# Kernel optimization log

Hardware: AMD Instinct MI355X
Metric: run time of the kernel (lower is better)

## Reference

```python
import jax, jax.numpy as jnp
import numpy as np

H = 2048      # hidden_size
NH = 16       # num_heads
HD = H // NH  # attention_head_size = 128
NEG_BIAS = -10000.0


def setup_inputs() -> dict:
    key = jax.random.key(0)
    k1, k2, k3, k4, k5 = jax.random.split(key, 5)
    B, S = 2, 2048
    hidden_states = jax.random.normal(k1, (B, S, H), dtype=jnp.float32)
    scale = 1.0 / np.sqrt(H)
    w_qkv = jax.random.normal(k2, (H, 3 * H), dtype=jnp.float32) * scale
    b_qkv = jax.random.normal(k3, (3 * H,), dtype=jnp.float32) * 0.01
    w_out = jax.random.normal(k4, (H, H), dtype=jnp.float32) * scale
    b_out = jax.random.normal(k5, (H,), dtype=jnp.float32) * 0.01
    return {"hidden_states": hidden_states, "w_qkv": w_qkv, "b_qkv": b_qkv,
            "w_out": w_out, "b_out": b_out}


def reference(hidden_states, w_qkv, b_qkv, w_out, b_out):
    B, S, _ = hidden_states.shape
    # fused QKV projection -> [B, S, 3H]
    qkv = hidden_states @ w_qkv + b_qkv
    # split heads with 3*head_dim per head, then chunk (matches torch code)
    qkv = qkv.reshape(B, S, NH, 3 * HD).transpose(0, 2, 1, 3)  # [B, NH, S, 3*HD]
    q, k, v = jnp.split(qkv, 3, axis=-1)                       # each [B, NH, S, HD]
    # scaled scores [B, NH, S, S]
    scores = jnp.einsum('bhqd,bhkd->bhqk', q, k) / np.sqrt(HD)
    causal = jnp.tril(jnp.ones((S, S), dtype=bool))
    scores = jnp.where(causal[None, None], scores, jnp.float32(NEG_BIAS))
    probs = jax.nn.softmax(scores, axis=-1)
    ctx = jnp.einsum('bhqk,bhkd->bhqd', probs, v)  # [B, NH, S, HD]
    ctx = ctx.transpose(0, 2, 1, 3).reshape(B, S, H)
    return ctx @ w_out + b_out
```

## Files before the change

kernel.cpp:

```cpp
#include <hip/hip_runtime.h>
#include <hip/hip_bf16.h>

typedef __bf16 bf16x8 __attribute__((ext_vector_type(8)));
typedef float  f32x4  __attribute__((ext_vector_type(4)));

constexpr int   Bb   = 2;
constexpr int   Slen = 2048;
constexpr int   Hdim = 2048;
constexpr int   NHn  = 16;
constexpr int   HDd  = 128;
constexpr float QSCALE = 0.08838834764831845f;
constexpr float NEG    = -1e30f;

__device__ __forceinline__ void gld16(const __bf16* g, __bf16* l) {
    __builtin_amdgcn_global_load_lds(
        (__attribute__((address_space(1))) void*)(uintptr_t)(const void*)g,
        (__attribute__((address_space(3))) void*)l, 16, 0, 0);
}

__global__ __launch_bounds__(256) void cvt_bf16(const float* __restrict__ in,
                                                __bf16* __restrict__ out) {
    const size_t i = (size_t)(blockIdx.x * 256 + threadIdx.x) * 8;
    f32x4 a = *(const f32x4*)(in + i), b = *(const f32x4*)(in + i + 4);
    bf16x8 r;
    r[0] = (__bf16)a[0]; r[1] = (__bf16)a[1]; r[2] = (__bf16)a[2]; r[3] = (__bf16)a[3];
    r[4] = (__bf16)b[0]; r[5] = (__bf16)b[1]; r[6] = (__bf16)b[2]; r[7] = (__bf16)b[3];
    *(bf16x8*)(out + i) = r;
}

__global__ __launch_bounds__(256) void transpose_cvt(const float* __restrict__ in,
                                                     __bf16* __restrict__ out,
                                                     int R, int C) {
    __shared__ float t[64][65];
    const int c0 = blockIdx.x * 64, r0 = blockIdx.y * 64;
    const int tx = threadIdx.x & 63, ty = threadIdx.x >> 6;
#pragma unroll
    for (int i = 0; i < 16; ++i) {
        int r = i * 4 + ty;
        t[r][tx] = in[(size_t)(r0 + r) * C + c0 + tx];
    }
    __syncthreads();
#pragma unroll
    for (int i = 0; i < 16; ++i) {
        int r = i * 4 + ty;
        out[(size_t)(c0 + r) * R + r0 + tx] = (__bf16)t[tx][r];
    }
}


#define BAR    __builtin_amdgcn_s_barrier()
#define LGKM0  asm volatile("s_waitcnt lgkmcnt(0)" ::: "memory")
#define VMC(n) asm volatile("s_waitcnt vmcnt(" #n ")" ::: "memory")

#define STAGE(op, half, tt)                                                          \
  do {                                                                               \
    const int tt_ = (tt);                                                            \
    if (tt_ < NT) {                                                                  \
      __bf16* dst_ = lds + ((tt_ & 1) << 15) + ((op) << 14) + ((half) << 13);        \
      const __bf16* src_ = (op) ? Bt : A;                                            \
      const int rb_ = (op) ? n0 : m0;                                               \
      const int k0_ = tt_ << 6;                                                      \
      _Pragma("unroll")                                                              \
      for (int i_ = 0; i_ < 2; ++i_) {                                               \
        const int c_  = (i_ << 9) + tid;                                             \
        const int rl_ = c_ >> 3;                                                     \
        const int grow_ = rb_ + ((op) ? (((rl_ >> 5) << 6) + ((half) << 5) + (rl_ & 31)) \
                                      : (((rl_ >> 6) << 7) + ((half) << 6) + (rl_ & 63))); \
        const int gk_ = k0_ + (((c_ & 7) ^ (rl_ & 7)) << 3);                         \
        gld16(src_ + (size_t)grow_ * Kdim + gk_, dst_ + (c_ << 3));                  \
      }                                                                              \
    }                                                                                \
  } while (0)

#define LDA(bufv, mh)                                                                \
  do {                                                                               \
    const __bf16* Ab_ = lds + ((bufv) << 15) + ((mh) << 13) + (wg << 12) + (l16 << 6); \
    _Pragma("unroll")                                                                \
    for (int q_ = 0; q_ < 4; ++q_)                                                   \
      _Pragma("unroll")                                                              \
      for (int kk_ = 0; kk_ < 2; ++kk_)                                              \
        af[q_][kk_] = *(const bf16x8*)(Ab_ + (q_ << 10) +                            \
                        ((((kk_ << 2) + quad) ^ (l16 & 7)) << 3));                   \
  } while (0)

#define LDB(bufv, nh)                                                                \
  do {                                                                               \
    const __bf16* Bb_ = lds + ((bufv) << 15) + 16384 + ((nh) << 13) + (gn << 11) + (l16 << 6); \
    _Pragma("unroll")                                                                \
    for (int q_ = 0; q_ < 2; ++q_)                                                   \
      _Pragma("unroll")                                                              \
      for (int kk_ = 0; kk_ < 2; ++kk_)                                              \
        bfr[((nh) << 1) + q_][kk_] = *(const bf16x8*)(Bb_ + (q_ << 10) +             \
                        ((((kk_ << 2) + quad) ^ (l16 & 7)) << 3));                   \
  } while (0)

#define MM(mh, nh)                                                                   \
  do {                                                                               \
    _Pragma("unroll")                                                                \
    for (int q_ = 0; q_ < 4; ++q_)                                                   \
      _Pragma("unroll")                                                              \
      for (int n_ = 0; n_ < 2; ++n_)                                                 \
        _Pragma("unroll")                                                            \
        for (int kk_ = 0; kk_ < 2; ++kk_)                                            \
          acc[((mh) << 2) + q_][((nh) << 1) + n_] =                                  \
            __builtin_amdgcn_mfma_f32_16x16x32_bf16(                                 \
              af[q_][kk_], bfr[((nh) << 1) + n_][kk_],                               \
              acc[((mh) << 2) + q_][((nh) << 1) + n_], 0, 0, 0);                     \
  } while (0)

template <int MODE>
__global__ __launch_bounds__(512, 2) void gemm8(
    const __bf16* __restrict__ A, const __bf16* __restrict__ Bt,
    const float* __restrict__ bias, int Kdim, int Ndim,
    float* __restrict__ Cout,
    __bf16* __restrict__ Qo, __bf16* __restrict__ Ko, __bf16* __restrict__ Vto) {
    __shared__ __bf16 lds[65536];
    const int tid  = threadIdx.x;
    const int lane = tid & 63, wave = tid >> 6;
    const int quad = lane >> 4, l16 = lane & 15;
    const int wg = wave >> 2;
    const int gn = wave & 3;
    const int m0 = blockIdx.y * 256, n0 = blockIdx.x * 256;
    const int NT = Kdim >> 6;

    f32x4  acc[8][4] = {};
    bf16x8 af[4][2];
    bf16x8 bfr[4][2];

    STAGE(0, 0, 0); STAGE(1, 0, 0); STAGE(1, 1, 0); STAGE(0, 1, 0);
    STAGE(0, 0, 1); STAGE(1, 0, 1); STAGE(1, 1, 1);
    VMC(6);
    BAR;

    for (int t = 0; t < NT; ++t) {
        const int cb = t & 1;
        LDA(cb, 0); LDB(cb, 0);
        STAGE(0, 1, t + 1);
        BAR; LGKM0;
        __builtin_amdgcn_s_setprio(1); MM(0, 0); __builtin_amdgcn_s_setprio(0);
        BAR;
        LDB(cb, 1);
        STAGE(0, 0, t + 2);
        BAR; LGKM0;
        __builtin_amdgcn_s_setprio(1); MM(0, 1); __builtin_amdgcn_s_setprio(0);
        BAR;
        LDA(cb, 1);
        STAGE(1, 0, t + 2);
        BAR; LGKM0;
        __builtin_amdgcn_s_setprio(1); MM(1, 1); __builtin_amdgcn_s_setprio(0);
        BAR;
        STAGE(1, 1, t + 2);
        if (t < NT - 2) { VMC(6); } else { VMC(0); }
        BAR;
        __builtin_amdgcn_s_setprio(1); MM(1, 0); __builtin_amdgcn_s_setprio(0);
        BAR;
    }

#pragma unroll
    for (int mi = 0; mi < 8; ++mi) {
#pragma unroll
        for (int r = 0; r < 4; ++r) {
            const int m = m0 + wg * 128 + (mi >> 2) * 64 + (mi & 3) * 16 + quad * 4 + r;
            const int b = m >> 11, s = m & 2047;
#pragma unroll
            for (int ni = 0; ni < 4; ++ni) {
                const int cc = n0 + gn * 64 + (ni >> 1) * 32 + (ni & 1) * 16 + l16;
                float val = acc[mi][ni][r] + bias[cc];
                if (MODE == 1) {
                    Cout[(size_t)m * Ndim + cc] = val;
                } else {
                    const int h = cc / 384;
                    const int rr = cc - h * 384;
                    const size_t hb = ((size_t)(b * NHn + h) * Slen + s);
                    if (rr < 128)
                        Qo[hb * HDd + rr] = (__bf16)(val * QSCALE);
                    else if (rr < 256)
                        Ko[hb * HDd + (rr - 128)] = (__bf16)val;
                    else
                        Vto[((size_t)(b * NHn + h) * HDd + (rr - 256)) * Slen + s] = (__bf16)val;
                }
            }
        }
    }
}


#define ASTAGE(tt)                                                                   \
  do {                                                                               \
    const int tt_ = (tt);                                                            \
    if (tt_ < ktiles) {                                                              \
      const int kb_ = tt_ << 6;                                                      \
      __bf16* kd_ = Ks + ((tt_ & 1) << 13);                                          \
      __bf16* vd_ = Vs + ((tt_ & 1) << 13);                                          \
      _Pragma("unroll")                                                              \
      for (int i_ = 0; i_ < 2; ++i_) {                                               \
        const int c_ = (i_ << 9) + tid;                        \
        const int kr_ = c_ >> 4, kc_ = c_ & 15;           \
        gld16(Kb + (size_t)(kb_ + kr_) * HDd + ((kc_ ^ (kr_ & 7)) << 3),             \
              kd_ + (c_ << 3));                                                      \
        const int vr_ = c_ >> 3, vc_ = c_ & 7;               \
        gld16(Vb + (size_t)vr_ * Slen + kb_ + ((vc_ ^ (vr_ & 7)) << 3),              \
              vd_ + (c_ << 3));                                                      \
      }                                                                              \
    }                                                                                \
  } while (0)

__global__ __launch_bounds__(512, 4) void attn_k(const __bf16* __restrict__ Q,
                                                 const __bf16* __restrict__ Kmat,
                                                 const __bf16* __restrict__ Vt,
                                                 __bf16* __restrict__ ctx) {
    __shared__ __bf16 Ks[2 * 64 * 128];
    __shared__ __bf16 Vs[2 * 128 * 64];
    __shared__ __bf16 Ps[8 * 16 * 64];
    const int tid = threadIdx.x, lane = tid & 63, wave = tid >> 6;
    const int quad = lane >> 4, l16 = lane & 15;
    const int bh = blockIdx.y;
    const int qt = gridDim.x - 1 - blockIdx.x;
    const int b = bh >> 4, h = bh & 15;
    const __bf16* Qb = Q    + (size_t)bh * Slen * HDd;
    const __bf16* Kb = Kmat + (size_t)bh * Slen * HDd;
    const __bf16* Vb = Vt   + (size_t)bh * HDd * Slen;
    const int q0 = qt * 128;
    const int qa = q0 + wave * 16 + l16;
    const int qc = q0 + wave * 16 + quad * 4;
    const int swz = (l16 & 7);

    bf16x8 qf[4];
#pragma unroll
    for (int kk = 0; kk < 4; ++kk)
        qf[kk] = *(const bf16x8*)(Qb + (size_t)qa * HDd + kk * 32 + quad * 8);

    f32x4 accO[8] = {};
    float m_i[4] = {NEG, NEG, NEG, NEG};
    float l_i[4] = {0.f, 0.f, 0.f, 0.f};
    __bf16* Pw = Ps + wave * 1024;

    const int ktiles = 2 * qt + 2;

    ASTAGE(0);
    for (int kt = 0; kt < ktiles; ++kt) {
        const int cur = kt & 1;
        const int kb0 = kt * 64;
        ASTAGE(kt + 1);
        if (kt + 1 < ktiles) { VMC(4); } else { VMC(0); }
        BAR;

        const __bf16* Kt = Ks + (cur << 13);
        const __bf16* Vc = Vs + (cur << 13);

        f32x4 sc[4];
#pragma unroll
        for (int nk = 0; nk < 4; ++nk) {
            f32x4 z = {0.f, 0.f, 0.f, 0.f};
#pragma unroll
            for (int kk = 0; kk < 4; ++kk) {
                bf16x8 kf = *(const bf16x8*)(Kt + (nk * 16 + l16) * 128 +
                                             (((kk << 2) + quad) ^ swz) * 8);
                z = __builtin_amdgcn_mfma_f32_16x16x32_bf16(qf[kk], kf, z, 0, 0, 0);
            }
            sc[nk] = z;
        }
        if (kt >= ktiles - 2) {
#pragma unroll
            for (int nk = 0; nk < 4; ++nk) {
                const int kg = kb0 + nk * 16 + l16;
#pragma unroll
                for (int r = 0; r < 4; ++r)
                    if (kg > qc + r) sc[nk][r] = NEG;
            }
        }
#pragma unroll
        for (int r = 0; r < 4; ++r) {
            float mm = fmaxf(fmaxf(sc[0][r], sc[1][r]), fmaxf(sc[2][r], sc[3][r]));
            mm = fmaxf(mm, __shfl_xor(mm, 1));
            mm = fmaxf(mm, __shfl_xor(mm, 2));
            mm = fmaxf(mm, __shfl_xor(mm, 4));
            mm = fmaxf(mm, __shfl_xor(mm, 8));
            const float mnew = fmaxf(m_i[r], mm);
            const float alpha = __expf(m_i[r] - mnew);
            float ls = 0.f;
#pragma unroll
            for (int nk = 0; nk < 4; ++nk) {
                float p = __expf(sc[nk][r] - mnew);
                sc[nk][r] = p;
                ls += p;
            }
            ls += __shfl_xor(ls, 1);
            ls += __shfl_xor(ls, 2);
            ls += __shfl_xor(ls, 4);
            ls += __shfl_xor(ls, 8);
            l_i[r] = l_i[r] * alpha + ls;
            m_i[r] = mnew;
#pragma unroll
            for (int nd = 0; nd < 8; ++nd) accO[nd][r] *= alpha;
        }

#pragma unroll
        for (int nk = 0; nk < 4; ++nk)
#pragma unroll
            for (int r = 0; r < 4; ++r) {
                const int row = quad * 4 + r, col = nk * 16 + l16;
                Pw[row * 64 + (((col >> 3) ^ (row & 7)) << 3) + (col & 7)] =
                    (__bf16)sc[nk][r];
            }
        bf16x8 pf[2];
#pragma unroll
        for (int kk = 0; kk < 2; ++kk)
            pf[kk] = *(const bf16x8*)(Pw + l16 * 64 + ((((kk << 2) + quad) ^ swz) << 3));

#pragma unroll
        for (int nd = 0; nd < 8; ++nd)
#pragma unroll
            for (int kk = 0; kk < 2; ++kk) {
                bf16x8 vf = *(const bf16x8*)(Vc + (nd * 16 + l16) * 64 +
                                             ((((kk << 2) + quad) ^ swz) << 3));
                accO[nd] = __builtin_amdgcn_mfma_f32_16x16x32_bf16(pf[kk], vf, accO[nd], 0, 0, 0);
            }
        LGKM0;
        BAR;
    }

#pragma unroll
    for (int nd = 0; nd < 8; ++nd)
#pragma unroll
        for (int r = 0; r < 4; ++r) {
            const int s = q0 + wave * 16 + quad * 4 + r;
            const int d = nd * 16 + l16;
            const float o = accO[nd][r] / fmaxf(l_i[r], 1e-20f);
            ctx[((size_t)b * Slen + s) * Hdim + h * HDd + d] = (__bf16)o;
        }
}

extern "C" void kernel_launch(void* const* d_in, const int* in_sizes, int n_in,
                              void* d_out, int out_size, void* d_ws, size_t ws_size,
                              hipStream_t stream) {
    const float* hs   = (const float*)d_in[0];
    const float* wqkv = (const float*)d_in[1];
    const float* bqkv = (const float*)d_in[2];
    const float* wout = (const float*)d_in[3];
    const float* bout = (const float*)d_in[4];
    float* out = (float*)d_out;

    __bf16* ws    = (__bf16*)d_ws;
    __bf16* wqkvT = ws;
    __bf16* woutT = wqkvT + (size_t)6144 * 2048;
    __bf16* Qs    = woutT + (size_t)2048 * 2048;
    __bf16* Kms   = Qs  + (size_t)Bb * NHn * Slen * HDd;
    __bf16* Vts   = Kms + (size_t)Bb * NHn * Slen * HDd;
    __bf16* ctx   = Vts + (size_t)Bb * NHn * Slen * HDd;
    __bf16* hsb   = ctx;

    cvt_bf16<<<(Bb * Slen * Hdim) / (256 * 8), 256, 0, stream>>>(hs, hsb);
    transpose_cvt<<<dim3(6144 / 64, 2048 / 64), 256, 0, stream>>>(wqkv, wqkvT, 2048, 6144);
    transpose_cvt<<<dim3(2048 / 64, 2048 / 64), 256, 0, stream>>>(wout, woutT, 2048, 2048);
    gemm8<0><<<dim3(6144 / 256, 4096 / 256), 512, 0, stream>>>(
        hsb, wqkvT, bqkv, Hdim, 3 * Hdim, nullptr, Qs, Kms, Vts);
    attn_k<<<dim3(Slen / 128, Bb * NHn), 512, 0, stream>>>(Qs, Kms, Vts, ctx);
    gemm8<1><<<dim3(2048 / 256, 4096 / 256), 512, 0, stream>>>(
        ctx, woutT, bout, Hdim, Hdim, out, nullptr, nullptr, nullptr);
}
```

Measured before the change: 477.9 us.

## Remap block indices for XCD-aware locality and pin scheduling around barriers

Both the GEMM and attention kernels remap the flat block index so that consecutive logical tiles are grouped onto the same XCD (stride-8 interleave). The aim is better L2 reuse of shared A/B or K/V tiles. Scheduling barriers are added around the waitcnt/barrier points so the compiler cannot move loads or MFMAs across them, and s_setprio is raised around the attention MFMA blocks. The GEMM remap hardcodes by=nf&15, so it assumes a 16-row grid and could mis-index other shapes. The attention remap hardcodes 16 q-tiles and 512 blocks.

```diff
diff --git a/kernel.cpp b/kernel.cpp
--- a/kernel.cpp
+++ b/kernel.cpp
@@ -51,6 +51,7 @@
 #define BAR    __builtin_amdgcn_s_barrier()
 #define LGKM0  asm volatile("s_waitcnt lgkmcnt(0)" ::: "memory")
 #define VMC(n) asm volatile("s_waitcnt vmcnt(" #n ")" ::: "memory")
+#define SCHED0 __builtin_amdgcn_sched_barrier(0)
 
 #define STAGE(op, half, tt)                                                          \
   do {                                                                               \
@@ -120,7 +121,12 @@
     const int quad = lane >> 4, l16 = lane & 15;
     const int wg = wave >> 2;
     const int gn = wave & 3;
-    const int m0 = blockIdx.y * 256, n0 = blockIdx.x * 256;
+
+    const int flat = blockIdx.x + blockIdx.y * gridDim.x;
+    const int cpx  = (gridDim.x * gridDim.y) >> 3;
+    const int nf   = (flat & 7) * cpx + (flat >> 3);
+    const int bx   = nf >> 4, by = nf & 15;
+    const int m0 = by * 256, n0 = bx * 256;
     const int NT = Kdim >> 6;
 
     f32x4  acc[8][4] = {};
@@ -129,6 +135,7 @@
 
     STAGE(0, 0, 0); STAGE(1, 0, 0); STAGE(1, 1, 0); STAGE(0, 1, 0);
     STAGE(0, 0, 1); STAGE(1, 0, 1); STAGE(1, 1, 1);
+    SCHED0;
     VMC(6);
     BAR;
 
@@ -136,20 +143,24 @@
         const int cb = t & 1;
         LDA(cb, 0); LDB(cb, 0);
         STAGE(0, 1, t + 1);
-        BAR; LGKM0;
+        SCHED0;
+        BAR; LGKM0; SCHED0;
         __builtin_amdgcn_s_setprio(1); MM(0, 0); __builtin_amdgcn_s_setprio(0);
         BAR;
         LDB(cb, 1);
         STAGE(0, 0, t + 2);
-        BAR; LGKM0;
+        SCHED0;
+        BAR; LGKM0; SCHED0;
         __builtin_amdgcn_s_setprio(1); MM(0, 1); __builtin_amdgcn_s_setprio(0);
         BAR;
         LDA(cb, 1);
         STAGE(1, 0, t + 2);
-        BAR; LGKM0;
+        SCHED0;
+        BAR; LGKM0; SCHED0;
         __builtin_amdgcn_s_setprio(1); MM(1, 1); __builtin_amdgcn_s_setprio(0);
         BAR;
         STAGE(1, 1, t + 2);
+        SCHED0;
         if (t < NT - 2) { VMC(6); } else { VMC(0); }
         BAR;
         __builtin_amdgcn_s_setprio(1); MM(1, 0); __builtin_amdgcn_s_setprio(0);
@@ -214,8 +225,11 @@
     __shared__ __bf16 Ps[8 * 16 * 64];
     const int tid = threadIdx.x, lane = tid & 63, wave = tid >> 6;
     const int quad = lane >> 4, l16 = lane & 15;
-    const int bh = blockIdx.y;
-    const int qt = gridDim.x - 1 - blockIdx.x;
+
+    const int flat = blockIdx.x + (blockIdx.y << 4);
+    const int nf   = (flat & 7) * 64 + (flat >> 3);
+    const int qx   = nf & 15, bh = nf >> 4;
+    const int qt   = 15 - qx;
     const int b = bh >> 4, h = bh & 15;
     const __bf16* Qb = Q    + (size_t)bh * Slen * HDd;
     const __bf16* Kb = Kmat + (size_t)bh * Slen * HDd;
@@ -242,6 +256,7 @@
         const int cur = kt & 1;
         const int kb0 = kt * 64;
         ASTAGE(kt + 1);
+        SCHED0;
         if (kt + 1 < ktiles) { VMC(4); } else { VMC(0); }
         BAR;
 
@@ -249,6 +264,7 @@
         const __bf16* Vc = Vs + (cur << 13);
 
         f32x4 sc[4];
+        __builtin_amdgcn_s_setprio(1);
 #pragma unroll
         for (int nk = 0; nk < 4; ++nk) {
             f32x4 z = {0.f, 0.f, 0.f, 0.f};
@@ -260,6 +276,7 @@
             }
             sc[nk] = z;
         }
+        __builtin_amdgcn_s_setprio(0);
         if (kt >= ktiles - 2) {
 #pragma unroll
             for (int nk = 0; nk < 4; ++nk) {
@@ -308,6 +325,7 @@
         for (int kk = 0; kk < 2; ++kk)
             pf[kk] = *(const bf16x8*)(Pw + l16 * 64 + ((((kk << 2) + quad) ^ swz) << 3));
 
+        __builtin_amdgcn_s_setprio(1);
 #pragma unroll
         for (int nd = 0; nd < 8; ++nd)
 #pragma unroll
@@ -316,7 +334,8 @@
                                              ((((kk << 2) + quad) ^ swz) << 3));
                 accO[nd] = __builtin_amdgcn_mfma_f32_16x16x32_bf16(pf[kk], vf, accO[nd], 0, 0, 0);
             }
-        LGKM0;
+        __builtin_amdgcn_s_setprio(0);
+        LGKM0; SCHED0;
         BAR;
     }
 
```

Result: faster. 466.5 us (-2.4%).
